# Performance work log

Hardware: AMD Instinct MI355X
Metric: run time of the kernel (lower is better)

## Reference

```python
import jax, jax.numpy as jnp
import numpy as np

N, D, DB, E, H = 1024, 512, 64, 32768, 1024

def setup_inputs() -> dict:
    key = jax.random.key(0)
    k = jax.random.split(key, 6)
    object_feats = jax.random.normal(k[0], (N, D), dtype=jnp.float32)
    bboxes_embedding = jax.random.normal(k[1], (N, N, DB), dtype=jnp.float32)
    pairs = jax.random.randint(k[2], (E, 2), 0, N, dtype=jnp.int64)
    # Kaiming-normal-ish init for the two Linear layers
    W1 = jax.random.normal(k[3], (D + D + DB, H), dtype=jnp.float32) * np.sqrt(2.0 / (D + D + DB))
    b1 = jnp.zeros((H,), dtype=jnp.float32)
    W2 = jax.random.normal(k[4], (H, D), dtype=jnp.float32) * np.sqrt(2.0 / H)
    b2 = jnp.zeros((D,), dtype=jnp.float32)
    return {"object_feats": object_feats, "bboxes_embedding": bboxes_embedding,
            "pairs": pairs, "W1": W1, "b1": b1, "W2": W2, "b2": b2}

def reference(object_feats, bboxes_embedding, pairs, W1, b1, W2, b2):
    sub = pairs[:, 0]
    obj = pairs[:, 1]
    # gather pair features: [E, D] each, plus pairwise bbox embedding [E, DB]
    f_sub = object_feats[sub]
    f_obj = object_feats[obj]
    bb = bboxes_embedding[sub, obj]
    x = jnp.concatenate((f_sub, f_obj, bb), axis=1)  # [E, 2D+DB]
    h = jax.nn.relu(x @ W1 + b1)
    out = h @ W2 + b2  # [E, D]
    n = object_feats.shape[0]
    # scatter-mean into subject nodes; each node's own feature is included once,
    # so new_feat[i] = (object_feats[i] + sum_{pairs with sub==i} out) / (1 + count[i]).
    # Nodes with no incident pairs keep their original feature (count==0 -> identity).
    seg_sum = jax.ops.segment_sum(out, sub, num_segments=n)  # [N, D]
    count = jax.ops.segment_sum(jnp.ones((out.shape[0],), dtype=out.dtype), sub, num_segments=n)
    new_feats = (object_feats + seg_sum) / (1.0 + count)[:, None]
    return (new_feats, bboxes_embedding, pairs)
```

## Files before the change

### kernel.cpp

```cpp
#include <hip/hip_runtime.h>

#define N_OBJ 1024
#define E_P   32768

typedef float f32x4 __attribute__((ext_vector_type(4)));
typedef short bf16x8 __attribute__((ext_vector_type(8)));
typedef unsigned short u16x4 __attribute__((ext_vector_type(4)));

__device__ __forceinline__ unsigned short f2bf(float f) {
    unsigned u = __float_as_uint(f);
    u = u + 0x7FFFu + ((u >> 16) & 1u);
    return (unsigned short)(u >> 16);
}
__device__ __forceinline__ float bf2f(unsigned short u) {
    return __uint_as_float(((unsigned)u) << 16);
}

#define OFF_A    0
#define LEN_A    5242880
#define OFF_B    (OFF_A + LEN_A)
#define LEN_B    4194304
#define OFF_SEG  (OFF_B + LEN_B)
#define LEN_SEG  4194304
#define OFF_OUT  (OFF_SEG + LEN_SEG)
#define LEN_OUT  3145728

__device__ __forceinline__ void copy_nt(const f32x4* __restrict__ src,
                                        f32x4* __restrict__ dst,
                                        int off, int len, int nb, int cb) {
    int stride = nb * 256;
    int i = off + cb * 256 + threadIdx.x;
    int end = off + len;
    for (; i + 3 * stride < end; i += 4 * stride) {
        f32x4 v0 = __builtin_nontemporal_load(&src[i]);
        f32x4 v1 = __builtin_nontemporal_load(&src[i + stride]);
        f32x4 v2 = __builtin_nontemporal_load(&src[i + 2 * stride]);
        f32x4 v3 = __builtin_nontemporal_load(&src[i + 3 * stride]);
        __builtin_nontemporal_store(v0, &dst[i]);
        __builtin_nontemporal_store(v1, &dst[i + stride]);
        __builtin_nontemporal_store(v2, &dst[i + 2 * stride]);
        __builtin_nontemporal_store(v3, &dst[i + 3 * stride]);
    }
    for (; i < end; i += stride) {
        f32x4 a = __builtin_nontemporal_load(&src[i]);
        __builtin_nontemporal_store(a, &dst[i]);
    }
}

__global__ __launch_bounds__(256) void k_zero(int* __restrict__ counts) {
    ((int4*)counts)[threadIdx.x] = make_int4(0, 0, 0, 0);
}

__global__ __launch_bounds__(256) void k_a(const float* __restrict__ W1,
                                           const float* __restrict__ W2,
                                           const float* __restrict__ feats,
                                           const int* __restrict__ pairs,
                                           unsigned short* __restrict__ w1pqT,
                                           unsigned short* __restrict__ w1cT,
                                           unsigned short* __restrict__ w2T,
                                           unsigned short* __restrict__ featsb,
                                           float* __restrict__ out_pairs,
                                           int* __restrict__ counts,
                                           int* __restrict__ rank,
                                           const f32x4* __restrict__ csrc,
                                           f32x4* __restrict__ cdst) {
    int bid = blockIdx.x, tid = threadIdx.x;
    if ((bid % 3) == 2) { copy_nt(csrc, cdst, OFF_A, LEN_A, 1056, bid / 3); return; }
    int job = (bid / 3) * 2 + (bid % 3);
    if (job >= 1856) {
        int i = (job - 1856) * 256 + tid;
        out_pairs[i] = (float)pairs[i];
        if (i < E_P) rank[i] = atomicAdd(&counts[pairs[2 * i]], 1);
        return;
    }
    if (job >= 1600) {
        int base = (job - 1600) * 2048 + tid * 8;
        float4 v0 = *(const float4*)&feats[base];
        float4 v1 = *(const float4*)&feats[base + 4];
        u16x4 o0 = { f2bf(v0.x), f2bf(v0.y), f2bf(v0.z), f2bf(v0.w) };
        u16x4 o1 = { f2bf(v1.x), f2bf(v1.y), f2bf(v1.z), f2bf(v1.w) };
        *(u16x4*)&featsb[base] = o0;
        *(u16x4*)&featsb[base + 4] = o1;
        return;
    }
    const float* in; unsigned short* out;
    int LDI, LDO, r0, c0, nbase, kbase;
    if (job < 1024) {
        r0 = (job >> 5) * 32; c0 = (job & 31) * 32;
        in = W1; LDI = 1024; out = w1pqT; LDO = 512;
        nbase = c0 + (r0 >= 512 ? 1024 : 0); kbase = r0 & 511;
    } else if (job < 1088) {
        int t = job - 1024; r0 = 1024 + (t >> 5) * 32; c0 = (t & 31) * 32;
        in = W1; LDI = 1024; out = w1cT; LDO = 64;
        nbase = c0; kbase = r0 - 1024;
    } else {
        int t = job - 1088; r0 = (t >> 4) * 32; c0 = (t & 15) * 32;
        in = W2; LDI = 512; out = w2T; LDO = 1024;
        nbase = c0; kbase = r0;
    }
    __shared__ float lds[32][33];
    int ti = tid >> 3, tj = (tid & 7) * 4;
    float4 v = *(const float4*)&in[(size_t)(r0 + ti) * LDI + c0 + tj];
    lds[ti][tj] = v.x; lds[ti][tj + 1] = v.y; lds[ti][tj + 2] = v.z; lds[ti][tj + 3] = v.w;
    __syncthreads();
    int oc = tid >> 3, oj = (tid & 7) * 4;
    u16x4 o = { f2bf(lds[oj][oc]), f2bf(lds[oj + 1][oc]),
                f2bf(lds[oj + 2][oc]), f2bf(lds[oj + 3][oc]) };
    *(u16x4*)&out[(size_t)(nbase + oc) * LDO + kbase + oj] = o;
}

__global__ __launch_bounds__(256) void k_b(const int* __restrict__ counts,
                                           const int* __restrict__ rank,
                                           const int* __restrict__ pairs,
                                           const float* __restrict__ bb,
                                           int* __restrict__ csr_obj,
                                           unsigned short* __restrict__ bbgc,
                                           int* __restrict__ offsets,
                                           const unsigned short* __restrict__ featsb,
                                           const unsigned short* __restrict__ w1pqT,
                                           const float* __restrict__ b1,
                                           float* __restrict__ P,
                                           unsigned short* __restrict__ Qb,
                                           const f32x4* __restrict__ csrc,
                                           f32x4* __restrict__ cdst) {
    int bid = blockIdx.x, tid = threadIdx.x;
    if ((bid % 3) < 2) { copy_nt(csrc, cdst, OFF_B, LEN_B, 1282, (bid / 3) * 2 + (bid % 3)); return; }
    int role = bid / 3;

    if (role >= 129) {
        int job = role - 129;
        int m0 = (job >> 5) * 64, n0 = (job & 31) * 64;
        int w = tid >> 6, l = tid & 63;
        int ln = l & 15, kb = (l >> 4) * 8;
        int row = m0 + w * 16 + ln;
        f32x4 acc[4] = {};
        for (int k0 = 0; k0 < 512; k0 += 32) {
            bf16x8 a = *(const bf16x8*)&featsb[(size_t)row * 512 + k0 + kb];
            #pragma unroll
            for (int f = 0; f < 4; ++f) {
                bf16x8 b = *(const bf16x8*)&w1pqT[(size_t)(n0 + f * 16 + ln) * 512 + k0 + kb];
                acc[f] = __builtin_amdgcn_mfma_f32_16x16x32_bf16(a, b, acc[f], 0, 0, 0);
            }
        }
        int mr = m0 + w * 16 + (l >> 4) * 4;
        if (n0 < 1024) {
            #pragma unroll
            for (int f = 0; f < 4; ++f) {
                int n = n0 + f * 16 + ln;
                float b1v = b1[n];
                #pragma unroll
                for (int r = 0; r < 4; ++r)
                    P[(size_t)(mr + r) * 1024 + n] = acc[f][r] + b1v;
            }
        } else {
            #pragma unroll
            for (int f = 0; f < 4; ++f) {
                int n = n0 - 1024 + f * 16 + ln;
                #pragma unroll
                for (int r = 0; r < 4; ++r)
                    Qb[(size_t)(mr + r) * 1024 + n] = f2bf(acc[f][r]);
            }
        }
        return;
    }

    __shared__ int sbuf[2][256];
    __shared__ int soff[1024];
    int c[4]; int s = 0;
    #pragma unroll
    for (int i = 0; i < 4; ++i) { c[i] = counts[tid * 4 + i]; s += c[i]; }
    sbuf[0][tid] = s;
    __syncthreads();
    int sel = 0;
    for (int d = 1; d < 256; d <<= 1) {
        int v = sbuf[sel][tid];
        if (tid >= d) v += sbuf[sel][tid - d];
        sbuf[sel ^ 1][tid] = v;
        sel ^= 1;
        __syncthreads();
    }
    int base = sbuf[sel][tid] - s;
    int run = base;
    #pragma unroll
    for (int i = 0; i < 4; ++i) { soff[tid * 4 + i] = run; run += c[i]; }
    __syncthreads();

    if (role == 0) {
        #pragma unroll
        for (int i = 0; i < 4; ++i) offsets[tid * 4 + i] = soff[tid * 4 + i];
        return;
    }

    int e = (role - 1) * 256 + tid;
    int sub = pairs[2 * e];
    int obj = pairs[2 * e + 1];
    int pos = soff[sub] + rank[e];
    csr_obj[pos] = obj;
    const f32x4* src = (const f32x4*)&bb[((size_t)sub * 1024 + (size_t)obj) * 64];
    u16x4* dst = (u16x4*)&bbgc[(size_t)pos * 64];
    #pragma unroll
    for (int i = 0; i < 16; ++i) {
        f32x4 v = __builtin_nontemporal_load(&src[i]);
        u16x4 o = { f2bf(v.x), f2bf(v.y), f2bf(v.z), f2bf(v.w) };
        dst[i] = o;
    }
}

__global__ __launch_bounds__(256) void k_seg(const int* __restrict__ csr_obj,
                                             const int* __restrict__ offsets,
                                             const int* __restrict__ counts,
                                             const unsigned short* __restrict__ bbgc,
                                             const unsigned short* __restrict__ w1cT,
                                             const float* __restrict__ P,
                                             const unsigned short* __restrict__ Qb,
                                             float* __restrict__ HS,
                                             const f32x4* __restrict__ csrc,
                                             f32x4* __restrict__ cdst) {
    int bid = blockIdx.x, tid = threadIdx.x;
    int x = bid & 7, k = bid >> 3;
    if (k >= 512) { copy_nt(csrc, cdst, OFF_SEG, LEN_SEG, 2048, (k - 512) * 8 + x); return; }
    const int qd = x >> 1;
    const int seg = k * 2 + (x & 1);
    const int start = offsets[seg];
    const int n = counts[seg];

    const int w = tid >> 6, l = tid & 63;
    const int ln = l & 15, g4 = l >> 4, kb = g4 * 8;
    const int cbase = qd * 256;
    const int wbase = cbase + w * 64;

    __shared__ unsigned short qs[32][264];

    float pv[4];
    #pragma unroll
    for (int f = 0; f < 4; ++f)
        pv[f] = P[(size_t)seg * 1024 + wbase + f * 16 + ln];

    float hpart[4] = {0.f, 0.f, 0.f, 0.f};

    for (int c0 = 0; c0 < n; c0 += 32) {
        int m = n - c0; if (m > 32) m = 32;
        const int mA = m < 16 ? m : 16;
        const int mB = m - 16;

        __syncthreads();
        {
            int p = tid >> 3, j = tid & 7;
            if (p < m) {
                int op = csr_obj[start + c0 + p];
                const uint4* qrow = (const uint4*)&Qb[(size_t)op * 1024 + cbase];
                #pragma unroll
                for (int i = 0; i < 4; ++i) {
                    uint4 v = qrow[j * 4 + i];
                    *(uint4*)&qs[p][(j * 4 + i) * 8] = v;
                }
            }
        }

        int iA = start + c0 + (ln < mA ? ln : mA - 1);
        int iB = (mB > 0) ? (start + c0 + 16 + (ln < mB ? ln : mB - 1)) : iA;
        const unsigned short* brA = &bbgc[(size_t)iA * 64];
        const unsigned short* brB = &bbgc[(size_t)iB * 64];
        bf16x8 A0a = *(const bf16x8*)&brA[kb];
        bf16x8 A1a = *(const bf16x8*)&brA[32 + kb];
        bf16x8 A0b = *(const bf16x8*)&brB[kb];
        bf16x8 A1b = *(const bf16x8*)&brB[32 + kb];

        bool vA0 = (g4 * 4 + 0) < mA, vA1 = (g4 * 4 + 1) < mA;
        bool vA2 = (g4 * 4 + 2) < mA, vA3 = (g4 * 4 + 3) < mA;
        bool vB0 = (g4 * 4 + 0) < mB, vB1 = (g4 * 4 + 1) < mB;
        bool vB2 = (g4 * 4 + 2) < mB, vB3 = (g4 * 4 + 3) < mB;

        __syncthreads();

        #pragma unroll
        for (int f = 0; f < 4; ++f) {
            int col = wbase + f * 16 + ln;
            int cc = col - cbase;
            const unsigned short* wr = &w1cT[(size_t)col * 64];
            bf16x8 b0 = *(const bf16x8*)&wr[kb];
            bf16x8 b1 = *(const bf16x8*)&wr[32 + kb];
            f32x4 dA = {0.f, 0.f, 0.f, 0.f};
            dA = __builtin_amdgcn_mfma_f32_16x16x32_bf16(A0a, b0, dA, 0, 0, 0);
            dA = __builtin_amdgcn_mfma_f32_16x16x32_bf16(A1a, b1, dA, 0, 0, 0);
            f32x4 dB = {0.f, 0.f, 0.f, 0.f};
            dB = __builtin_amdgcn_mfma_f32_16x16x32_bf16(A0b, b0, dB, 0, 0, 0);
            dB = __builtin_amdgcn_mfma_f32_16x16x32_bf16(A1b, b1, dB, 0, 0, 0);
            float qA0 = bf2f(qs[g4 * 4 + 0][cc]);
            float qA1 = bf2f(qs[g4 * 4 + 1][cc]);
            float qA2 = bf2f(qs[g4 * 4 + 2][cc]);
            float qA3 = bf2f(qs[g4 * 4 + 3][cc]);
            float qB0 = bf2f(qs[16 + g4 * 4 + 0][cc]);
            float qB1 = bf2f(qs[16 + g4 * 4 + 1][cc]);
            float qB2 = bf2f(qs[16 + g4 * 4 + 2][cc]);
            float qB3 = bf2f(qs[16 + g4 * 4 + 3][cc]);
            float h = 0.f;
            h += vA0 ? fmaxf(dA[0] + pv[f] + qA0, 0.f) : 0.f;
            h += vA1 ? fmaxf(dA[1] + pv[f] + qA1, 0.f) : 0.f;
            h += vA2 ? fmaxf(dA[2] + pv[f] + qA2, 0.f) : 0.f;
            h += vA3 ? fmaxf(dA[3] + pv[f] + qA3, 0.f) : 0.f;
            h += vB0 ? fmaxf(dB[0] + pv[f] + qB0, 0.f) : 0.f;
            h += vB1 ? fmaxf(dB[1] + pv[f] + qB1, 0.f) : 0.f;
            h += vB2 ? fmaxf(dB[2] + pv[f] + qB2, 0.f) : 0.f;
            h += vB3 ? fmaxf(dB[3] + pv[f] + qB3, 0.f) : 0.f;
            hpart[f] += h;
        }
    }

    #pragma unroll
    for (int f = 0; f < 4; ++f) {
        float h = hpart[f];
        h += __shfl_xor(h, 16);
        h += __shfl_xor(h, 32);
        if (l < 16) HS[(size_t)seg * 1024 + wbase + f * 16 + l] = h;
    }
}

__global__ __launch_bounds__(256) void k_out(const float* __restrict__ HS,
                                             const unsigned short* __restrict__ w2T,
                                             const float* __restrict__ feats,
                                             const float* __restrict__ b2,
                                             const int* __restrict__ counts,
                                             float* __restrict__ out0,
                                             const f32x4* __restrict__ csrc,
                                             f32x4* __restrict__ cdst) {
    int bid = blockIdx.x;
    if ((bid % 17) != 16) { copy_nt(csrc, cdst, OFF_OUT, LEN_OUT, 2048, (bid / 17) * 16 + (bid % 17)); return; }
    int job = bid / 17;
    int m0 = (job >> 3) * 64, n0 = (job & 7) * 64;
    int tid = threadIdx.x, w = tid >> 6, l = tid & 63;
    int ln = l & 15, kb = (l >> 4) * 8;
    int row = m0 + w * 16 + ln;
    f32x4 acc[4] = {};
    for (int k0 = 0; k0 < 1024; k0 += 32) {
        const float* hp = &HS[(size_t)row * 1024 + k0 + kb];
        float4 h0 = *(const float4*)&hp[0];
        float4 h1 = *(const float4*)&hp[4];
        bf16x8 a;
        a[0] = (short)f2bf(h0.x); a[1] = (short)f2bf(h0.y); a[2] = (short)f2bf(h0.z); a[3] = (short)f2bf(h0.w);
        a[4] = (short)f2bf(h1.x); a[5] = (short)f2bf(h1.y); a[6] = (short)f2bf(h1.z); a[7] = (short)f2bf(h1.w);
        #pragma unroll
        for (int f = 0; f < 4; ++f) {
            bf16x8 b = *(const bf16x8*)&w2T[(size_t)(n0 + f * 16 + ln) * 1024 + k0 + kb];
            acc[f] = __builtin_amdgcn_mfma_f32_16x16x32_bf16(a, b, acc[f], 0, 0, 0);
        }
    }
    int mr = m0 + w * 16 + (l >> 4) * 4;
    float cv[4], inv[4];
    #pragma unroll
    for (int r = 0; r < 4; ++r) {
        float c = (float)counts[mr + r];
        cv[r] = c;
        inv[r] = 1.0f / (1.0f + c);
    }
    #pragma unroll
    for (int f = 0; f < 4; ++f) {
        int n = n0 + f * 16 + ln;
        float b2v = b2[n];
        #pragma unroll
        for (int r = 0; r < 4; ++r) {
            float fv = feats[(size_t)(mr + r) * 512 + n];
            out0[(size_t)(mr + r) * 512 + n] = (fv + acc[f][r] + cv[r] * b2v) * inv[r];
        }
    }
}

extern "C" void kernel_launch(void* const* d_in, const int* in_sizes, int n_in,
                              void* d_out, int out_size, void* d_ws, size_t ws_size,
                              hipStream_t stream) {
    const float* feats = (const float*)d_in[0];
    const float* bb    = (const float*)d_in[1];
    const int*   pairs = (const int*)d_in[2];
    const float* W1    = (const float*)d_in[3];
    const float* b1    = (const float*)d_in[4];
    const float* W2    = (const float*)d_in[5];
    const float* b2    = (const float*)d_in[6];

    float* out        = (float*)d_out;
    float* out_feats  = out;
    float* out_bb     = out + (size_t)N_OBJ * 512;
    float* out_pairs  = out + (size_t)N_OBJ * 512 + (size_t)N_OBJ * N_OBJ * 64;

    char* w = (char*)d_ws;
    unsigned short* featsb = (unsigned short*)w;
    unsigned short* w1pqT  = (unsigned short*)(w + (1u << 20));
    unsigned short* w1cT   = (unsigned short*)(w + (3u << 20));
    unsigned short* w2T    = (unsigned short*)(w + (3u << 20) + (128u << 10));
    float*          HS     = (float*)(w + (4u << 20) + (128u << 10));
    float*          P      = (float*)(w + (8u << 20) + (128u << 10));
    unsigned short* Qb     = (unsigned short*)(w + (12u << 20) + (128u << 10));
    unsigned short* bbgc   = (unsigned short*)(w + (14u << 20) + (128u << 10));
    char* ints = w + (18u << 20) + (128u << 10);
    int*      counts  = (int*)ints;
    int*      offsets = (int*)(ints + 4096);
    int*      csr_obj = (int*)(ints + 8192);
    int*      rank    = (int*)(ints + 8192 + 131072);

    const f32x4* cbb  = (const f32x4*)bb;
    f32x4*       cobb = (f32x4*)out_bb;

    k_zero<<<1, 256, 0, stream>>>(counts);

    k_a<<<3168, 256, 0, stream>>>(W1, W2, feats, pairs, w1pqT, w1cT, w2T, featsb,
                                  out_pairs, counts, rank, cbb, cobb);
    k_b<<<1923, 256, 0, stream>>>(counts, rank, pairs, bb, csr_obj, bbgc, offsets,
                                  featsb, w1pqT, b1, P, Qb, cbb, cobb);
    k_seg<<<6144, 256, 0, stream>>>(csr_obj, offsets, counts, bbgc, w1cT, P, Qb, HS,
                                    cbb, cobb);
    k_out<<<2176, 256, 0, stream>>>(HS, w2T, feats, b2, counts, out_feats, cbb, cobb);
}
```

Before: 215.8 us.

## Move bbox-embedding passthrough copy out of compute kernels into standalone kernel

Removes the non-temporal copy of the 256 MB bbox embedding that was spread as extra blocks across the four compute kernels. It is replaced by one dedicated copy kernel launched after all compute, and the compute kernels are launched only with their own blocks. This simplifies indexing and may let the copy reach full bandwidth without competing with compute. The cost is that the copy no longer overlaps with the compute stages, so its time adds serially to the total.

```diff
diff --git a/kernel.cpp b/kernel.cpp
--- a/kernel.cpp
+++ b/kernel.cpp
@@ -16,39 +16,20 @@
     return __uint_as_float(((unsigned)u) << 16);
 }
 
-#define OFF_A    0
-#define LEN_A    5242880
-#define OFF_B    (OFF_A + LEN_A)
-#define LEN_B    4194304
-#define OFF_SEG  (OFF_B + LEN_B)
-#define LEN_SEG  4194304
-#define OFF_OUT  (OFF_SEG + LEN_SEG)
-#define LEN_OUT  3145728
-
-__device__ __forceinline__ void copy_nt(const f32x4* __restrict__ src,
-                                        f32x4* __restrict__ dst,
-                                        int off, int len, int nb, int cb) {
-    int stride = nb * 256;
-    int i = off + cb * 256 + threadIdx.x;
-    int end = off + len;
-    for (; i + 3 * stride < end; i += 4 * stride) {
-        f32x4 v0 = __builtin_nontemporal_load(&src[i]);
-        f32x4 v1 = __builtin_nontemporal_load(&src[i + stride]);
-        f32x4 v2 = __builtin_nontemporal_load(&src[i + 2 * stride]);
-        f32x4 v3 = __builtin_nontemporal_load(&src[i + 3 * stride]);
-        __builtin_nontemporal_store(v0, &dst[i]);
-        __builtin_nontemporal_store(v1, &dst[i + stride]);
-        __builtin_nontemporal_store(v2, &dst[i + 2 * stride]);
-        __builtin_nontemporal_store(v3, &dst[i + 3 * stride]);
-    }
-    for (; i < end; i += stride) {
-        f32x4 a = __builtin_nontemporal_load(&src[i]);
-        __builtin_nontemporal_store(a, &dst[i]);
-    }
-}
-
 __global__ __launch_bounds__(256) void k_zero(int* __restrict__ counts) {
     ((int4*)counts)[threadIdx.x] = make_int4(0, 0, 0, 0);
+}
+
+__global__ __launch_bounds__(256) void k_copy(const f32x4* __restrict__ src,
+                                              f32x4* __restrict__ dst) {
+    int i = blockIdx.x * 256 + threadIdx.x;
+    const int stride = 8192 * 256;
+    #pragma unroll
+    for (int it = 0; it < 8; ++it) {
+        f32x4 v = __builtin_nontemporal_load(&src[i]);
+        __builtin_nontemporal_store(v, &dst[i]);
+        i += stride;
+    }
 }
 
 __global__ __launch_bounds__(256) void k_a(const float* __restrict__ W1,
@@ -61,12 +42,8 @@
                                            unsigned short* __restrict__ featsb,
                                            float* __restrict__ out_pairs,
                                            int* __restrict__ counts,
-                                           int* __restrict__ rank,
-                                           const f32x4* __restrict__ csrc,
-                                           f32x4* __restrict__ cdst) {
-    int bid = blockIdx.x, tid = threadIdx.x;
-    if ((bid % 3) == 2) { copy_nt(csrc, cdst, OFF_A, LEN_A, 1056, bid / 3); return; }
-    int job = (bid / 3) * 2 + (bid % 3);
+                                           int* __restrict__ rank) {
+    int job = blockIdx.x, tid = threadIdx.x;
     if (job >= 1856) {
         int i = (job - 1856) * 256 + tid;
         out_pairs[i] = (float)pairs[i];
@@ -120,12 +97,8 @@
                                            const unsigned short* __restrict__ w1pqT,
                                            const float* __restrict__ b1,
                                            float* __restrict__ P,
-                                           unsigned short* __restrict__ Qb,
-                                           const f32x4* __restrict__ csrc,
-                                           f32x4* __restrict__ cdst) {
-    int bid = blockIdx.x, tid = threadIdx.x;
-    if ((bid % 3) < 2) { copy_nt(csrc, cdst, OFF_B, LEN_B, 1282, (bid / 3) * 2 + (bid % 3)); return; }
-    int role = bid / 3;
+                                           unsigned short* __restrict__ Qb) {
+    int role = blockIdx.x, tid = threadIdx.x;
 
     if (role >= 129) {
         int job = role - 129;
@@ -213,12 +186,9 @@
                                              const unsigned short* __restrict__ w1cT,
                                              const float* __restrict__ P,
                                              const unsigned short* __restrict__ Qb,
-                                             float* __restrict__ HS,
-                                             const f32x4* __restrict__ csrc,
-                                             f32x4* __restrict__ cdst) {
+                                             float* __restrict__ HS) {
     int bid = blockIdx.x, tid = threadIdx.x;
     int x = bid & 7, k = bid >> 3;
-    if (k >= 512) { copy_nt(csrc, cdst, OFF_SEG, LEN_SEG, 2048, (k - 512) * 8 + x); return; }
     const int qd = x >> 1;
     const int seg = k * 2 + (x & 1);
     const int start = offsets[seg];
@@ -321,12 +291,8 @@
                                              const float* __restrict__ feats,
                                              const float* __restrict__ b2,
                                              const int* __restrict__ counts,
-                                             float* __restrict__ out0,
-                                             const f32x4* __restrict__ csrc,
-                                             f32x4* __restrict__ cdst) {
-    int bid = blockIdx.x;
-    if ((bid % 17) != 16) { copy_nt(csrc, cdst, OFF_OUT, LEN_OUT, 2048, (bid / 17) * 16 + (bid % 17)); return; }
-    int job = bid / 17;
+                                             float* __restrict__ out0) {
+    int job = blockIdx.x;
     int m0 = (job >> 3) * 64, n0 = (job & 7) * 64;
     int tid = threadIdx.x, w = tid >> 6, l = tid & 63;
     int ln = l & 15, kb = (l >> 4) * 8;
@@ -396,16 +362,14 @@
     int*      csr_obj = (int*)(ints + 8192);
     int*      rank    = (int*)(ints + 8192 + 131072);
 
-    const f32x4* cbb  = (const f32x4*)bb;
-    f32x4*       cobb = (f32x4*)out_bb;
-
     k_zero<<<1, 256, 0, stream>>>(counts);
 
-    k_a<<<3168, 256, 0, stream>>>(W1, W2, feats, pairs, w1pqT, w1cT, w2T, featsb,
-                                  out_pairs, counts, rank, cbb, cobb);
-    k_b<<<1923, 256, 0, stream>>>(counts, rank, pairs, bb, csr_obj, bbgc, offsets,
-                                  featsb, w1pqT, b1, P, Qb, cbb, cobb);
-    k_seg<<<6144, 256, 0, stream>>>(csr_obj, offsets, counts, bbgc, w1cT, P, Qb, HS,
-                                    cbb, cobb);
-    k_out<<<2176, 256, 0, stream>>>(HS, w2T, feats, b2, counts, out_feats, cbb, cobb);
-}
+    k_a<<<2112, 256, 0, stream>>>(W1, W2, feats, pairs, w1pqT, w1cT, w2T, featsb,
+                                  out_pairs, counts, rank);
+    k_b<<<641, 256, 0, stream>>>(counts, rank, pairs, bb, csr_obj, bbgc, offsets,
+                                 featsb, w1pqT, b1, P, Qb);
+    k_seg<<<4096, 256, 0, stream>>>(csr_obj, offsets, counts, bbgc, w1cT, P, Qb, HS);
+    k_out<<<128, 256, 0, stream>>>(HS, w2T, feats, b2, counts, out_feats);
+
+    k_copy<<<8192, 256, 0, stream>>>((const f32x4*)bb, (f32x4*)out_bb);
+}
```

Result: slower. 241.0 us (+11.7%).
